# Kernel optimization log

Hardware: AMD Instinct MI355X
Metric: run time of the kernel (lower is better)

The kernel has to match this reference:

```python
import jax, jax.numpy as jnp
import numpy as np

TAU = 2.0      # LIF membrane time constant
ALPHA = 4.0    # spikingjelly surrogate.Sigmoid default alpha
EPS = 1e-5     # BatchNorm eps
HEADS = 8

@jax.custom_vjp
def heaviside(x):
    return (x >= 0).astype(x.dtype)

def _hv_fwd(x):
    return (x >= 0).astype(x.dtype), x

def _hv_bwd(x, g):
    s = jax.nn.sigmoid(ALPHA * x)
    return (g * ALPHA * s * (1.0 - s),)

heaviside.defvjp(_hv_fwd, _hv_bwd)

def lif(x, vth=1.0):
    # multi-step LIF, decay_input=True, v_reset=0 (hard reset), detach_reset=True
    def step(v, xt):
        v = v + (xt - v) / TAU
        s = heaviside(v - vth)
        v = v * (1.0 - jax.lax.stop_gradient(s))
        return v, s
    _, spikes = jax.lax.scan(step, jnp.zeros_like(x[0]), x)
    return spikes

def bn(x, gamma, beta, mean, var):
    # x: [T,B,C,N]; eval-mode BatchNorm1d over channel axis 2
    inv = gamma * jax.lax.rsqrt(var + EPS)
    return x * inv[None, None, :, None] + (beta - mean * inv)[None, None, :, None]

def conv1x1(x, w):
    # x: [T,B,C,N], w: [Cout,Cin] (Conv1d kernel_size=1)
    return jnp.einsum('tbcn,dc->tbdn', x, w)

def setup_inputs():
    key = jax.random.key(0)
    ks = jax.random.split(key, 24)
    T, B, C, H, W = 4, 16, 512, 32, 32
    scale = 1.0 / np.sqrt(C)
    d = {}
    d['x'] = jax.random.normal(ks[0], (T, B, C, H, W), jnp.float32)
    def bn_params(i):
        g = 1.0 + 0.1 * jax.random.normal(ks[i], (C,), jnp.float32)
        b = 0.1 * jax.random.normal(ks[i + 1], (C,), jnp.float32)
        m = 0.1 * jax.random.normal(ks[i + 2], (C,), jnp.float32)
        v = jax.random.uniform(ks[i + 3], (C,), jnp.float32, 0.5, 1.5)
        return g, b, m, v
    d['q_w'] = scale * jax.random.normal(ks[1], (C, C), jnp.float32)
    d['q_gamma'], d['q_beta'], d['q_mean'], d['q_var'] = bn_params(2)
    d['k_w'] = scale * jax.random.normal(ks[6], (C, C), jnp.float32)
    d['k_gamma'], d['k_beta'], d['k_mean'], d['k_var'] = bn_params(7)
    d['proj_w'] = scale * jax.random.normal(ks[11], (C, C), jnp.float32)
    d['proj_b'] = 0.01 * jax.random.normal(ks[12], (C,), jnp.float32)
    d['p_gamma'], d['p_beta'], d['p_mean'], d['p_var'] = bn_params(13)
    return d

def reference(x, q_w, q_gamma, q_beta, q_mean, q_var,
              k_w, k_gamma, k_beta, k_mean, k_var,
              proj_w, proj_b, p_gamma, p_beta, p_mean, p_var):
    T, B, C, H, W = x.shape
    N = H * W
    Dh = C // HEADS
    xs = lif(x).reshape(T, B, C, N)                    # shortcut_lif then flatten(3)
    q = lif(bn(conv1x1(xs, q_w), q_gamma, q_beta, q_mean, q_var))
    k = lif(bn(conv1x1(xs, k_w), k_gamma, k_beta, k_mean, k_var))
    qh = q.reshape(T, B, HEADS, Dh, N).sum(axis=3, keepdims=True)  # [T,B,h,1,N]
    attn = lif(qh, vth=0.5)
    kh = k.reshape(T, B, HEADS, Dh, N)
    y = (attn * kh).reshape(T, B, C, N)
    y = bn(conv1x1(y, proj_w) + proj_b[None, None, :, None],
           p_gamma, p_beta, p_mean, p_var)
    return y.reshape(T, B, C, H, W), attn
```

## Files before the change

### kernel.cpp

```cpp
#include <hip/hip_runtime.h>

typedef unsigned short u16;
typedef unsigned int u32;
typedef float f32x4 __attribute__((ext_vector_type(4)));
typedef short s16x8 __attribute__((ext_vector_type(8)));

#define T_ 4
#define B_ 16
#define C_ 512
#define N_ 1024
#define YSZ 33554432

__device__ __forceinline__ u16 f2bf(float f) {
  u32 u = __float_as_uint(f);
  u32 r = u + 0x7FFFu + ((u >> 16) & 1u);
  return (u16)(r >> 16);
}
__device__ __forceinline__ float bf2f(u16 h) { return __uint_as_float(((u32)h) << 16); }

__device__ __forceinline__ void async16(const void* g, void* l) {
  __builtin_amdgcn_global_load_lds((const __attribute__((address_space(1))) void*)g,
                                   (__attribute__((address_space(3))) void*)l, 16, 0, 0);
}

__global__ void prep_kernel(const float* __restrict__ qw, const float* __restrict__ kw,
                            const float* __restrict__ pw,
                            const float* __restrict__ qg, const float* __restrict__ qb,
                            const float* __restrict__ qm, const float* __restrict__ qv,
                            const float* __restrict__ kg, const float* __restrict__ kb,
                            const float* __restrict__ km, const float* __restrict__ kv,
                            const float* __restrict__ pg, const float* __restrict__ pbt,
                            const float* __restrict__ pm, const float* __restrict__ pv,
                            u16* __restrict__ whlq, u16* __restrict__ whlk,
                            u16* __restrict__ pwb, float* __restrict__ consts) {
  int blk = blockIdx.x, tid = threadIdx.x;
  if (blk < 512) {
    int d = blk;
    for (int c = tid; c < 512; c += 256) {
      float w = qw[d * 512 + c];
      u16 hi = f2bf(w);
      whlq[d * 1024 + c] = hi;
      whlq[d * 1024 + 512 + c] = f2bf(w - bf2f(hi));
      w = kw[d * 512 + c];
      hi = f2bf(w);
      whlk[d * 1024 + c] = hi;
      whlk[d * 1024 + 512 + c] = f2bf(w - bf2f(hi));
      pwb[d * 512 + c] = f2bf(pw[d * 512 + c]);
    }
  } else {
    for (int c = tid; c < 512; c += 256) {
      float inv = qg[c] / sqrtf(qv[c] + 1e-5f);
      consts[c] = inv; consts[512 + c] = qb[c] - qm[c] * inv;
      inv = kg[c] / sqrtf(kv[c] + 1e-5f);
      consts[1024 + c] = inv; consts[1536 + c] = kb[c] - km[c] * inv;
      inv = pg[c] / sqrtf(pv[c] + 1e-5f);
      consts[2048 + c] = inv; consts[2560 + c] = pbt[c] - pm[c] * inv;
    }
  }
}

__global__ __launch_bounds__(256) void lifx_kernel(const float* __restrict__ x,
                                                   u16* __restrict__ xs) {
  int b = blockIdx.z;
  int cbase = blockIdx.y * 64, nbase = blockIdx.x * 64;
  int tid = threadIdx.x;
  int c_l = tid >> 6, n_l = tid & 63;
  __shared__ __align__(16) u16 tile[64 * 72];
  float v[16];
#pragma unroll
  for (int i = 0; i < 16; ++i) v[i] = 0.f;
  for (int t = 0; t < 4; ++t) {
    const float* xp = x + ((size_t)(t * 16 + b) * 512 + cbase + c_l * 16) * 1024 + nbase + n_l;
#pragma unroll
    for (int i = 0; i < 16; ++i) {
      float xv = xp[(size_t)i * 1024];
      float vn = v[i] + 0.5f * (xv - v[i]);
      bool s = vn >= 1.0f;
      tile[n_l * 72 + c_l * 16 + i] = s ? 0x3F80 : 0;
      v[i] = s ? 0.f : vn;
    }
    __syncthreads();
    u16* yb = xs + ((size_t)(t * 16 + b) * 1024 + nbase) * 512 + cbase;
#pragma unroll
    for (int e = 0; e < 2; ++e) {
      int chunk = tid * 2 + e;
      int n = chunk >> 3, c0 = (chunk & 7) * 8;
      *(uint4*)&yb[(size_t)n * 512 + c0] = *(const uint4*)&tile[n * 72 + c0];
    }
    __syncthreads();
  }
}

__global__ __launch_bounds__(256, 4) void gemm_q_kernel(
    const u16* __restrict__ A, const u16* __restrict__ Bbase,
    const float* __restrict__ consts, float* __restrict__ dout) {
  const int tid = threadIdx.x;
  const int lane = tid & 63, w = tid >> 6;
  const int quad = lane >> 4, l16 = lane & 15;
  const int b = blockIdx.z;
  const int m_blk = blockIdx.y * 64, n_blk = blockIdx.x * 128;
  const int srow = lane >> 3;
  const int scol = (((lane & 7) ^ srow) & 7) * 8;
  __shared__ __align__(16) u16 smem[2 * 4096 + 8192];
  u16* Ash = smem;
  u16* Asl = smem + 4096;
  u16* Bs  = smem + 8192;
  const int rxor = l16 & 7;
  float v[32];
#pragma unroll
  for (int i = 0; i < 32; ++i) v[i] = 0.f;
  float va[2] = {0.f, 0.f};

  for (int t = 0; t < 4; ++t) {
    f32x4 acc[4][2];
    const f32x4 zero = {0.f, 0.f, 0.f, 0.f};
#pragma unroll
    for (int i = 0; i < 4; ++i)
#pragma unroll
      for (int j = 0; j < 2; ++j) acc[i][j] = zero;
    const u16* Bt = Bbase + (size_t)(t * 16 + b) * (N_ * C_);

    for (int k0 = 0; k0 < 512; k0 += 64) {
#pragma unroll
      for (int i = 0; i < 2; ++i) {
        int r = i * 32 + w * 8 + srow;
        int lo = (i * 32 + w * 8) * 64;
        async16(A + (size_t)(m_blk + r) * 1024 + k0 + scol, &Ash[lo]);
        async16(A + (size_t)(m_blk + r) * 1024 + 512 + k0 + scol, &Asl[lo]);
      }
#pragma unroll
      for (int i = 0; i < 4; ++i) {
        int r = i * 32 + w * 8 + srow;
        async16(Bt + (size_t)(n_blk + r) * 512 + k0 + scol, &Bs[(i * 32 + w * 8) * 64]);
      }
      __syncthreads();
#pragma unroll
      for (int kk = 0; kk < 2; ++kk) {
        s16x8 ah[4], al[4], bf[2];
        const int slot = ((kk * 4 + quad) ^ rxor) * 8;
#pragma unroll
        for (int ti = 0; ti < 4; ++ti) {
          ah[ti] = *(const s16x8*)&Ash[(ti * 16 + l16) * 64 + slot];
          al[ti] = *(const s16x8*)&Asl[(ti * 16 + l16) * 64 + slot];
        }
#pragma unroll
        for (int tj = 0; tj < 2; ++tj)
          bf[tj] = *(const s16x8*)&Bs[(w * 32 + tj * 16 + l16) * 64 + slot];
#pragma unroll
        for (int ti = 0; ti < 4; ++ti)
#pragma unroll
          for (int tj = 0; tj < 2; ++tj) {
            acc[ti][tj] = __builtin_amdgcn_mfma_f32_16x16x32_bf16(ah[ti], bf[tj], acc[ti][tj], 0, 0, 0);
            acc[ti][tj] = __builtin_amdgcn_mfma_f32_16x16x32_bf16(al[ti], bf[tj], acc[ti][tj], 0, 0, 0);
          }
      }
      __syncthreads();
    }

    float qp[2] = {0.f, 0.f};
#pragma unroll
    for (int ti = 0; ti < 4; ++ti) {
#pragma unroll
      for (int r = 0; r < 4; ++r) {
        int row = m_blk + ti * 16 + quad * 4 + r;
        float iv = consts[row], ib = consts[512 + row];
#pragma unroll
        for (int tj = 0; tj < 2; ++tj) {
          float bnv = acc[ti][tj][r] * iv + ib;
          float vv = v[(ti * 2 + tj) * 4 + r];
          float vn = vv + 0.5f * (bnv - vv);
          bool s = vn >= 1.0f;
          v[(ti * 2 + tj) * 4 + r] = s ? 0.f : vn;
          qp[tj] += s ? 1.f : 0.f;
        }
      }
    }
    int h = m_blk >> 6;
#pragma unroll
    for (int tj = 0; tj < 2; ++tj) {
      float q = qp[tj];
      q += __shfl_xor(q, 16, 64);
      q += __shfl_xor(q, 32, 64);
      float vn = va[tj] + 0.5f * (q - va[tj]);
      bool s = vn >= 0.5f;
      va[tj] = s ? 0.f : vn;
      if (quad == 0) {
        int col = n_blk + w * 32 + tj * 16 + l16;
        dout[(size_t)YSZ + ((size_t)(t * 16 + b) * 8 + h) * 1024 + col] = s ? 1.f : 0.f;
      }
    }
  }
}

__global__ __launch_bounds__(256, 4) void gemm_k_kernel(
    const u16* __restrict__ A, const u16* __restrict__ Bbase,
    const float* __restrict__ consts, const float* __restrict__ dout,
    u16* __restrict__ y) {
  const int tid = threadIdx.x;
  const int lane = tid & 63, w = tid >> 6;
  const int quad = lane >> 4, l16 = lane & 15;
  const int b = blockIdx.z;
  const int m_blk = blockIdx.y * 64, n_blk = blockIdx.x * 128;
  const int srow = lane >> 3;
  const int scol = (((lane & 7) ^ srow) & 7) * 8;
  __shared__ __align__(16) u16 smem[2 * 4096 + 8192];
  u16* Ash = smem;
  u16* Asl = smem + 4096;
  u16* Bs  = smem + 8192;
  u16* Ys  = smem;
  const int rxor = l16 & 7;
  float v[32];
#pragma unroll
  for (int i = 0; i < 32; ++i) v[i] = 0.f;

  for (int t = 0; t < 4; ++t) {
    f32x4 acc[4][2];
    const f32x4 zero = {0.f, 0.f, 0.f, 0.f};
#pragma unroll
    for (int i = 0; i < 4; ++i)
#pragma unroll
      for (int j = 0; j < 2; ++j) acc[i][j] = zero;
    const u16* Bt = Bbase + (size_t)(t * 16 + b) * (N_ * C_);

    for (int k0 = 0; k0 < 512; k0 += 64) {
#pragma unroll
      for (int i = 0; i < 2; ++i) {
        int r = i * 32 + w * 8 + srow;
        int lo = (i * 32 + w * 8) * 64;
        async16(A + (size_t)(m_blk + r) * 1024 + k0 + scol, &Ash[lo]);
        async16(A + (size_t)(m_blk + r) * 1024 + 512 + k0 + scol, &Asl[lo]);
      }
#pragma unroll
      for (int i = 0; i < 4; ++i) {
        int r = i * 32 + w * 8 + srow;
        async16(Bt + (size_t)(n_blk + r) * 512 + k0 + scol, &Bs[(i * 32 + w * 8) * 64]);
      }
      __syncthreads();
#pragma unroll
      for (int kk = 0; kk < 2; ++kk) {
        s16x8 ah[4], al[4], bf[2];
        const int slot = ((kk * 4 + quad) ^ rxor) * 8;
#pragma unroll
        for (int ti = 0; ti < 4; ++ti) {
          ah[ti] = *(const s16x8*)&Ash[(ti * 16 + l16) * 64 + slot];
          al[ti] = *(const s16x8*)&Asl[(ti * 16 + l16) * 64 + slot];
        }
#pragma unroll
        for (int tj = 0; tj < 2; ++tj)
          bf[tj] = *(const s16x8*)&Bs[(w * 32 + tj * 16 + l16) * 64 + slot];
#pragma unroll
        for (int ti = 0; ti < 4; ++ti)
#pragma unroll
          for (int tj = 0; tj < 2; ++tj) {
            acc[ti][tj] = __builtin_amdgcn_mfma_f32_16x16x32_bf16(ah[ti], bf[tj], acc[ti][tj], 0, 0, 0);
            acc[ti][tj] = __builtin_amdgcn_mfma_f32_16x16x32_bf16(al[ti], bf[tj], acc[ti][tj], 0, 0, 0);
          }
      }
      __syncthreads();
    }

    int h = m_blk >> 6;
    float at[2];
#pragma unroll
    for (int tj = 0; tj < 2; ++tj) {
      int col = n_blk + w * 32 + tj * 16 + l16;
      at[tj] = dout[(size_t)YSZ + ((size_t)(t * 16 + b) * 8 + h) * 1024 + col];
    }

#pragma unroll
    for (int ti = 0; ti < 4; ++ti) {
      u16 pk[2][4];
#pragma unroll
      for (int r = 0; r < 4; ++r) {
        int row = m_blk + ti * 16 + quad * 4 + r;
        float iv = consts[1024 + row], ib = consts[1536 + row];
#pragma unroll
        for (int tj = 0; tj < 2; ++tj) {
          float bnv = acc[ti][tj][r] * iv + ib;
          float vv = v[(ti * 2 + tj) * 4 + r];
          float vn = vv + 0.5f * (bnv - vv);
          bool s = vn >= 1.0f;
          v[(ti * 2 + tj) * 4 + r] = s ? 0.f : vn;
          pk[tj][r] = (s && at[tj] != 0.f) ? 0x3F80 : 0;
        }
      }
#pragma unroll
      for (int tj = 0; tj < 2; ++tj) {
        int n_loc = w * 32 + tj * 16 + l16;
        int c_loc = ti * 16 + quad * 4;
        u32 lo2 = (u32)pk[tj][0] | ((u32)pk[tj][1] << 16);
        u32 hi2 = (u32)pk[tj][2] | ((u32)pk[tj][3] << 16);
        uint2 pv2; pv2.x = lo2; pv2.y = hi2;
        *(uint2*)&Ys[n_loc * 68 + c_loc] = pv2;
      }
    }
    __syncthreads();
    u16* yb = y + ((size_t)(t * 16 + b) * 1024 + n_blk) * 512 + m_blk;
#pragma unroll
    for (int p = 0; p < 4; ++p) {
      int idx = p * 256 + tid;
      int rown = idx >> 3, ch = (idx & 7) * 8;
      *(uint4*)&yb[(size_t)rown * 512 + ch] = *(const uint4*)&Ys[rown * 68 + ch];
    }
    __syncthreads();
  }
}

__global__ __launch_bounds__(256, 3) void gemm_proj_kernel(
    const u16* __restrict__ A, const u16* __restrict__ Bbase,
    float* __restrict__ outP, const float* __restrict__ projb,
    const float* __restrict__ consts) {
  const int tid = threadIdx.x;
  const int lane = tid & 63, w = tid >> 6;
  const int wm = w >> 1, wn = w & 1;
  const int quad = lane >> 4, l16 = lane & 15;
  const int tb = blockIdx.z;
  const int m_blk = blockIdx.y * 128, n_blk = blockIdx.x * 128;
  const int srow = lane >> 3;
  const int scol = (((lane & 7) ^ srow) & 7) * 8;
  __shared__ __align__(16) u16 As[128 * 64];
  __shared__ __align__(16) u16 Bs[128 * 64];
  f32x4 acc[4][4];
  const f32x4 zero = {0.f, 0.f, 0.f, 0.f};
#pragma unroll
  for (int i = 0; i < 4; ++i)
#pragma unroll
    for (int j = 0; j < 4; ++j) acc[i][j] = zero;
  const u16* Bt = Bbase + (size_t)tb * (N_ * C_);
  const int rxor = l16 & 7;

  for (int k0 = 0; k0 < 512; k0 += 64) {
#pragma unroll
    for (int i = 0; i < 4; ++i) {
      int r = i * 32 + w * 8 + srow;
      async16(A + (size_t)(m_blk + r) * 512 + k0 + scol, &As[(i * 32 + w * 8) * 64]);
      async16(Bt + (size_t)(n_blk + r) * 512 + k0 + scol, &Bs[(i * 32 + w * 8) * 64]);
    }
    __syncthreads();
#pragma unroll
    for (int kk = 0; kk < 2; ++kk) {
      s16x8 af[4], bf[4];
      const int slot = ((kk * 4 + quad) ^ rxor) * 8;
#pragma unroll
      for (int ti = 0; ti < 4; ++ti)
        af[ti] = *(const s16x8*)&As[(wm * 64 + ti * 16 + l16) * 64 + slot];
#pragma unroll
      for (int tj = 0; tj < 4; ++tj)
        bf[tj] = *(const s16x8*)&Bs[(wn * 64 + tj * 16 + l16) * 64 + slot];
#pragma unroll
      for (int ti = 0; ti < 4; ++ti)
#pragma unroll
        for (int tj = 0; tj < 4; ++tj)
          acc[ti][tj] = __builtin_amdgcn_mfma_f32_16x16x32_bf16(af[ti], bf[tj], acc[ti][tj], 0, 0, 0);
    }
    __syncthreads();
  }

  const float* pinv = consts + 2048;
  const float* pb2 = consts + 2560;
  float* o = outP + (size_t)tb * (C_ * N_);
#pragma unroll
  for (int ti = 0; ti < 4; ++ti) {
    int row0 = m_blk + wm * 64 + ti * 16 + quad * 4;
#pragma unroll
    for (int r = 0; r < 4; ++r) {
      int row = row0 + r;
      float bi = projb[row], piv = pinv[row], pbi = pb2[row];
#pragma unroll
      for (int tj = 0; tj < 4; ++tj) {
        int col = n_blk + wn * 64 + tj * 16 + l16;
        o[(size_t)row * N_ + col] = (acc[ti][tj][r] + bi) * piv + pbi;
      }
    }
  }
}

extern "C" void kernel_launch(void* const* d_in, const int* in_sizes, int n_in,
                              void* d_out, int out_size, void* d_ws, size_t ws_size,
                              hipStream_t stream) {
  const float* x   = (const float*)d_in[0];
  const float* qw  = (const float*)d_in[1];
  const float* qg  = (const float*)d_in[2];
  const float* qb  = (const float*)d_in[3];
  const float* qm  = (const float*)d_in[4];
  const float* qv  = (const float*)d_in[5];
  const float* kw  = (const float*)d_in[6];
  const float* kg  = (const float*)d_in[7];
  const float* kb  = (const float*)d_in[8];
  const float* km  = (const float*)d_in[9];
  const float* kv  = (const float*)d_in[10];
  const float* pw  = (const float*)d_in[11];
  const float* pb  = (const float*)d_in[12];
  const float* pg  = (const float*)d_in[13];
  const float* pbt = (const float*)d_in[14];
  const float* pm  = (const float*)d_in[15];
  const float* pv  = (const float*)d_in[16];
  float* out = (float*)d_out;
  char* ws = (char*)d_ws;

  u16* xs       = (u16*)ws;
  u16* y2       = (u16*)(ws + 67108864);
  u16* whlq     = (u16*)(ws + 201326592);
  u16* whlk     = (u16*)(ws + 202375168);
  u16* pwb      = (u16*)(ws + 203423744);
  float* consts = (float*)(ws + 203948032);

  prep_kernel<<<513, 256, 0, stream>>>(qw, kw, pw, qg, qb, qm, qv, kg, kb, km, kv,
                                       pg, pbt, pm, pv, whlq, whlk, pwb, consts);
  lifx_kernel<<<dim3(16, 8, 16), 256, 0, stream>>>(x, xs);
  gemm_q_kernel<<<dim3(8, 8, 16), 256, 0, stream>>>(whlq, xs, consts, out);
  gemm_k_kernel<<<dim3(8, 8, 16), 256, 0, stream>>>(whlk, xs, consts, out, y2);
  gemm_proj_kernel<<<dim3(8, 4, 64), 256, 0, stream>>>(pwb, y2, out, pb, consts);
}
```

Measured before the change: 475.2 us.

## Store binary spike tensors as packed bitmasks and expand in registers

The intermediate spike tensors (shortcut LIF output and attention-gated k) are now stored as one bit per element instead of bf16, and each GEMM expands the bits into bf16 MFMA operands in registers instead of staging them through LDS. This removes the LDS transpose in the LIF kernel and cuts the intermediate global traffic by a factor of sixteen. In exchange, every fragment pays extra ALU for bit expansion, B-operand loads become small uncoalesced per-lane reads, and the Y staging stride changes to support bit packing.

```diff
diff --git a/kernel.cpp b/kernel.cpp
--- a/kernel.cpp
+++ b/kernel.cpp
@@ -1,5 +1,6 @@
 #include <hip/hip_runtime.h>
 
+typedef unsigned char u8;
 typedef unsigned short u16;
 typedef unsigned int u32;
 typedef float f32x4 __attribute__((ext_vector_type(4)));
@@ -21,6 +22,15 @@
 __device__ __forceinline__ void async16(const void* g, void* l) {
   __builtin_amdgcn_global_load_lds((const __attribute__((address_space(1))) void*)g,
                                    (__attribute__((address_space(3))) void*)l, 16, 0, 0);
+}
+
+__device__ __forceinline__ s16x8 expand8(u32 m) {
+  union { u32 w[4]; s16x8 v; } u;
+  u.w[0] = (m & 1u   ? 0x3F80u : 0u) | (m & 2u   ? 0x3F800000u : 0u);
+  u.w[1] = (m & 4u   ? 0x3F80u : 0u) | (m & 8u   ? 0x3F800000u : 0u);
+  u.w[2] = (m & 16u  ? 0x3F80u : 0u) | (m & 32u  ? 0x3F800000u : 0u);
+  u.w[3] = (m & 64u  ? 0x3F80u : 0u) | (m & 128u ? 0x3F800000u : 0u);
+  return u.v;
 }
 
 __global__ void prep_kernel(const float* __restrict__ qw, const float* __restrict__ kw,
@@ -60,39 +70,32 @@
 }
 
 __global__ __launch_bounds__(256) void lifx_kernel(const float* __restrict__ x,
-                                                   u16* __restrict__ xs) {
+                                                   u8* __restrict__ xsb) {
   int b = blockIdx.z;
   int cbase = blockIdx.y * 64, nbase = blockIdx.x * 64;
   int tid = threadIdx.x;
   int c_l = tid >> 6, n_l = tid & 63;
-  __shared__ __align__(16) u16 tile[64 * 72];
   float v[16];
 #pragma unroll
   for (int i = 0; i < 16; ++i) v[i] = 0.f;
   for (int t = 0; t < 4; ++t) {
     const float* xp = x + ((size_t)(t * 16 + b) * 512 + cbase + c_l * 16) * 1024 + nbase + n_l;
+    u32 mask = 0;
 #pragma unroll
     for (int i = 0; i < 16; ++i) {
       float xv = xp[(size_t)i * 1024];
       float vn = v[i] + 0.5f * (xv - v[i]);
       bool s = vn >= 1.0f;
-      tile[n_l * 72 + c_l * 16 + i] = s ? 0x3F80 : 0;
+      mask |= (s ? 1u : 0u) << i;
       v[i] = s ? 0.f : vn;
     }
-    __syncthreads();
-    u16* yb = xs + ((size_t)(t * 16 + b) * 1024 + nbase) * 512 + cbase;
-#pragma unroll
-    for (int e = 0; e < 2; ++e) {
-      int chunk = tid * 2 + e;
-      int n = chunk >> 3, c0 = (chunk & 7) * 8;
-      *(uint4*)&yb[(size_t)n * 512 + c0] = *(const uint4*)&tile[n * 72 + c0];
-    }
-    __syncthreads();
+    *(u16*)&xsb[((size_t)(t * 16 + b) * 1024 + nbase + n_l) * 64 + (cbase >> 3) + c_l * 2] =
+        (u16)mask;
   }
 }
 
 __global__ __launch_bounds__(256, 4) void gemm_q_kernel(
-    const u16* __restrict__ A, const u16* __restrict__ Bbase,
+    const u16* __restrict__ A, const u8* __restrict__ xsb,
     const float* __restrict__ consts, float* __restrict__ dout) {
   const int tid = threadIdx.x;
   const int lane = tid & 63, w = tid >> 6;
@@ -101,11 +104,12 @@
   const int m_blk = blockIdx.y * 64, n_blk = blockIdx.x * 128;
   const int srow = lane >> 3;
   const int scol = (((lane & 7) ^ srow) & 7) * 8;
-  __shared__ __align__(16) u16 smem[2 * 4096 + 8192];
+  __shared__ __align__(16) u16 smem[2 * 4096];
   u16* Ash = smem;
   u16* Asl = smem + 4096;
-  u16* Bs  = smem + 8192;
   const int rxor = l16 & 7;
+  const int row0 = n_blk + w * 32 + l16;
+  const int row1 = row0 + 16;
   float v[32];
 #pragma unroll
   for (int i = 0; i < 32; ++i) v[i] = 0.f;
@@ -118,7 +122,7 @@
     for (int i = 0; i < 4; ++i)
 #pragma unroll
       for (int j = 0; j < 2; ++j) acc[i][j] = zero;
-    const u16* Bt = Bbase + (size_t)(t * 16 + b) * (N_ * C_);
+    const u8* bitsT = xsb + (size_t)(t * 16 + b) * (N_ * 64);
 
     for (int k0 = 0; k0 < 512; k0 += 64) {
 #pragma unroll
@@ -128,11 +132,8 @@
         async16(A + (size_t)(m_blk + r) * 1024 + k0 + scol, &Ash[lo]);
         async16(A + (size_t)(m_blk + r) * 1024 + 512 + k0 + scol, &Asl[lo]);
       }
-#pragma unroll
-      for (int i = 0; i < 4; ++i) {
-        int r = i * 32 + w * 8 + srow;
-        async16(Bt + (size_t)(n_blk + r) * 512 + k0 + scol, &Bs[(i * 32 + w * 8) * 64]);
-      }
+      uint2 g0 = *(const uint2*)&bitsT[(size_t)row0 * 64 + (k0 >> 3)];
+      uint2 g1 = *(const uint2*)&bitsT[(size_t)row1 * 64 + (k0 >> 3)];
       __syncthreads();
 #pragma unroll
       for (int kk = 0; kk < 2; ++kk) {
@@ -143,9 +144,10 @@
           ah[ti] = *(const s16x8*)&Ash[(ti * 16 + l16) * 64 + slot];
           al[ti] = *(const s16x8*)&Asl[(ti * 16 + l16) * 64 + slot];
         }
-#pragma unroll
-        for (int tj = 0; tj < 2; ++tj)
-          bf[tj] = *(const s16x8*)&Bs[(w * 32 + tj * 16 + l16) * 64 + slot];
+        u32 w0 = kk ? g0.y : g0.x;
+        u32 w1 = kk ? g1.y : g1.x;
+        bf[0] = expand8((w0 >> (quad * 8)) & 0xFFu);
+        bf[1] = expand8((w1 >> (quad * 8)) & 0xFFu);
 #pragma unroll
         for (int ti = 0; ti < 4; ++ti)
 #pragma unroll
@@ -193,9 +195,9 @@
 }
 
 __global__ __launch_bounds__(256, 4) void gemm_k_kernel(
-    const u16* __restrict__ A, const u16* __restrict__ Bbase,
+    const u16* __restrict__ A, const u8* __restrict__ xsb,
     const float* __restrict__ consts, const float* __restrict__ dout,
-    u16* __restrict__ y) {
+    u8* __restrict__ y2b) {
   const int tid = threadIdx.x;
   const int lane = tid & 63, w = tid >> 6;
   const int quad = lane >> 4, l16 = lane & 15;
@@ -203,12 +205,13 @@
   const int m_blk = blockIdx.y * 64, n_blk = blockIdx.x * 128;
   const int srow = lane >> 3;
   const int scol = (((lane & 7) ^ srow) & 7) * 8;
-  __shared__ __align__(16) u16 smem[2 * 4096 + 8192];
+  __shared__ __align__(16) u16 smem[9216];
   u16* Ash = smem;
   u16* Asl = smem + 4096;
-  u16* Bs  = smem + 8192;
   u16* Ys  = smem;
   const int rxor = l16 & 7;
+  const int row0 = n_blk + w * 32 + l16;
+  const int row1 = row0 + 16;
   float v[32];
 #pragma unroll
   for (int i = 0; i < 32; ++i) v[i] = 0.f;
@@ -220,7 +223,7 @@
     for (int i = 0; i < 4; ++i)
 #pragma unroll
       for (int j = 0; j < 2; ++j) acc[i][j] = zero;
-    const u16* Bt = Bbase + (size_t)(t * 16 + b) * (N_ * C_);
+    const u8* bitsT = xsb + (size_t)(t * 16 + b) * (N_ * 64);
 
     for (int k0 = 0; k0 < 512; k0 += 64) {
 #pragma unroll
@@ -230,11 +233,8 @@
         async16(A + (size_t)(m_blk + r) * 1024 + k0 + scol, &Ash[lo]);
         async16(A + (size_t)(m_blk + r) * 1024 + 512 + k0 + scol, &Asl[lo]);
       }
-#pragma unroll
-      for (int i = 0; i < 4; ++i) {
-        int r = i * 32 + w * 8 + srow;
-        async16(Bt + (size_t)(n_blk + r) * 512 + k0 + scol, &Bs[(i * 32 + w * 8) * 64]);
-      }
+      uint2 g0 = *(const uint2*)&bitsT[(size_t)row0 * 64 + (k0 >> 3)];
+      uint2 g1 = *(const uint2*)&bitsT[(size_t)row1 * 64 + (k0 >> 3)];
       __syncthreads();
 #pragma unroll
       for (int kk = 0; kk < 2; ++kk) {
@@ -245,9 +245,10 @@
           ah[ti] = *(const s16x8*)&Ash[(ti * 16 + l16) * 64 + slot];
           al[ti] = *(const s16x8*)&Asl[(ti * 16 + l16) * 64 + slot];
         }
-#pragma unroll
-        for (int tj = 0; tj < 2; ++tj)
-          bf[tj] = *(const s16x8*)&Bs[(w * 32 + tj * 16 + l16) * 64 + slot];
+        u32 w0 = kk ? g0.y : g0.x;
+        u32 w1 = kk ? g1.y : g1.x;
+        bf[0] = expand8((w0 >> (quad * 8)) & 0xFFu);
+        bf[1] = expand8((w1 >> (quad * 8)) & 0xFFu);
 #pragma unroll
         for (int ti = 0; ti < 4; ++ti)
 #pragma unroll
@@ -291,23 +292,28 @@
         u32 lo2 = (u32)pk[tj][0] | ((u32)pk[tj][1] << 16);
         u32 hi2 = (u32)pk[tj][2] | ((u32)pk[tj][3] << 16);
         uint2 pv2; pv2.x = lo2; pv2.y = hi2;
-        *(uint2*)&Ys[n_loc * 68 + c_loc] = pv2;
+        *(uint2*)&Ys[n_loc * 72 + c_loc] = pv2;
       }
     }
     __syncthreads();
-    u16* yb = y + ((size_t)(t * 16 + b) * 1024 + n_blk) * 512 + m_blk;
+    u8* yb = y2b + ((size_t)(t * 16 + b) * 1024 + n_blk) * 64 + (m_blk >> 3);
 #pragma unroll
     for (int p = 0; p < 4; ++p) {
       int idx = p * 256 + tid;
-      int rown = idx >> 3, ch = (idx & 7) * 8;
-      *(uint4*)&yb[(size_t)rown * 512 + ch] = *(const uint4*)&Ys[rown * 68 + ch];
+      int rown = idx >> 3, bc = idx & 7;
+      uint4 q = *(const uint4*)&Ys[rown * 72 + bc * 8];
+      u32 byte = ((q.x >> 7) & 1u) | (((q.x >> 23) & 1u) << 1) |
+                 (((q.y >> 7) & 1u) << 2) | (((q.y >> 23) & 1u) << 3) |
+                 (((q.z >> 7) & 1u) << 4) | (((q.z >> 23) & 1u) << 5) |
+                 (((q.w >> 7) & 1u) << 6) | (((q.w >> 23) & 1u) << 7);
+      yb[(size_t)rown * 64 + bc] = (u8)byte;
     }
     __syncthreads();
   }
 }
 
 __global__ __launch_bounds__(256, 3) void gemm_proj_kernel(
-    const u16* __restrict__ A, const u16* __restrict__ Bbase,
+    const u16* __restrict__ A, const u8* __restrict__ y2b,
     float* __restrict__ outP, const float* __restrict__ projb,
     const float* __restrict__ consts) {
   const int tid = threadIdx.x;
@@ -319,23 +325,26 @@
   const int srow = lane >> 3;
   const int scol = (((lane & 7) ^ srow) & 7) * 8;
   __shared__ __align__(16) u16 As[128 * 64];
-  __shared__ __align__(16) u16 Bs[128 * 64];
   f32x4 acc[4][4];
   const f32x4 zero = {0.f, 0.f, 0.f, 0.f};
 #pragma unroll
   for (int i = 0; i < 4; ++i)
 #pragma unroll
     for (int j = 0; j < 4; ++j) acc[i][j] = zero;
-  const u16* Bt = Bbase + (size_t)tb * (N_ * C_);
+  const u8* bitsT = y2b + (size_t)tb * (N_ * 64);
   const int rxor = l16 & 7;
+  const int browb = n_blk + wn * 64 + l16;
 
   for (int k0 = 0; k0 < 512; k0 += 64) {
 #pragma unroll
     for (int i = 0; i < 4; ++i) {
       int r = i * 32 + w * 8 + srow;
       async16(A + (size_t)(m_blk + r) * 512 + k0 + scol, &As[(i * 32 + w * 8) * 64]);
-      async16(Bt + (size_t)(n_blk + r) * 512 + k0 + scol, &Bs[(i * 32 + w * 8) * 64]);
-    }
+    }
+    uint2 g[4];
+#pragma unroll
+    for (int tj = 0; tj < 4; ++tj)
+      g[tj] = *(const uint2*)&bitsT[(size_t)(browb + tj * 16) * 64 + (k0 >> 3)];
     __syncthreads();
 #pragma unroll
     for (int kk = 0; kk < 2; ++kk) {
@@ -345,8 +354,10 @@
       for (int ti = 0; ti < 4; ++ti)
         af[ti] = *(const s16x8*)&As[(wm * 64 + ti * 16 + l16) * 64 + slot];
 #pragma unroll
-      for (int tj = 0; tj < 4; ++tj)
-        bf[tj] = *(const s16x8*)&Bs[(wn * 64 + tj * 16 + l16) * 64 + slot];
+      for (int tj = 0; tj < 4; ++tj) {
+        u32 wbits = kk ? g[tj].y : g[tj].x;
+        bf[tj] = expand8((wbits >> (quad * 8)) & 0xFFu);
+      }
 #pragma unroll
       for (int ti = 0; ti < 4; ++ti)
 #pragma unroll
@@ -398,17 +409,17 @@
   float* out = (float*)d_out;
   char* ws = (char*)d_ws;
 
-  u16* xs       = (u16*)ws;
-  u16* y2       = (u16*)(ws + 67108864);
-  u16* whlq     = (u16*)(ws + 201326592);
-  u16* whlk     = (u16*)(ws + 202375168);
-  u16* pwb      = (u16*)(ws + 203423744);
-  float* consts = (float*)(ws + 203948032);
+  u8*  xsb      = (u8*)ws;
+  u8*  y2b      = (u8*)(ws + 4194304);
+  u16* whlq     = (u16*)(ws + 8388608);
+  u16* whlk     = (u16*)(ws + 9437184);
+  u16* pwb      = (u16*)(ws + 10485760);
+  float* consts = (float*)(ws + 11010048);
 
   prep_kernel<<<513, 256, 0, stream>>>(qw, kw, pw, qg, qb, qm, qv, kg, kb, km, kv,
                                        pg, pbt, pm, pv, whlq, whlk, pwb, consts);
-  lifx_kernel<<<dim3(16, 8, 16), 256, 0, stream>>>(x, xs);
-  gemm_q_kernel<<<dim3(8, 8, 16), 256, 0, stream>>>(whlq, xs, consts, out);
-  gemm_k_kernel<<<dim3(8, 8, 16), 256, 0, stream>>>(whlk, xs, consts, out, y2);
-  gemm_proj_kernel<<<dim3(8, 4, 64), 256, 0, stream>>>(pwb, y2, out, pb, consts);
-}
+  lifx_kernel<<<dim3(16, 8, 16), 256, 0, stream>>>(x, xsb);
+  gemm_q_kernel<<<dim3(8, 8, 16), 256, 0, stream>>>(whlq, xsb, consts, out);
+  gemm_k_kernel<<<dim3(8, 8, 16), 256, 0, stream>>>(whlk, xsb, consts, out, y2b);
+  gemm_proj_kernel<<<dim3(8, 4, 64), 256, 0, stream>>>(pwb, y2b, out, pb, consts);
+}
```

New measurement: 467.4 us. Within noise of the previous version (-1.7%).
